# Optimization experiments

Measured on AMD Instinct MI355X. Metric: run time of the kernel, lower is better.

The kernel has to match this reference:

```python
import jax, jax.numpy as jnp
from jax import lax
import numpy as np

B, C, Hf, Wf = 4, 256, 64, 64
COMP = max(C // 4, 16)  # 64
SCALE, K_UP, K_ENC = 2, 5, 3
EPS = 1e-5


def setup_inputs() -> dict:
    key = jax.random.key(0)
    ks = jax.random.split(key, 6)
    x = jax.random.normal(ks[0], (B, C, Hf, Wf), dtype=jnp.float32)
    w_comp = jax.random.normal(ks[1], (COMP, C), dtype=jnp.float32) * (1.0 / np.sqrt(C))
    bn_gamma = jnp.ones((COMP,), dtype=jnp.float32)
    bn_beta = jnp.zeros((COMP,), dtype=jnp.float32)
    bn_mean = jax.random.normal(ks[2], (COMP,), dtype=jnp.float32) * 0.1
    bn_var = jax.random.uniform(ks[3], (COMP,), dtype=jnp.float32, minval=0.5, maxval=1.5)
    w_enc = jax.random.normal(ks[4], (K_UP * K_UP * SCALE * SCALE, COMP, K_ENC, K_ENC), dtype=jnp.float32) * (1.0 / np.sqrt(COMP * K_ENC * K_ENC))
    return {"x": x, "w_comp": w_comp, "bn_gamma": bn_gamma, "bn_beta": bn_beta,
            "bn_mean": bn_mean, "bn_var": bn_var, "w_enc": w_enc}


def reference(x, w_comp, bn_gamma, bn_beta, bn_mean, bn_var, w_enc):
    b, c, h, w = x.shape
    s, k = SCALE, K_UP
    # 1x1 compression conv
    comp = jnp.einsum('bchw,oc->bohw', x, w_comp)
    # BatchNorm (eval-style, running stats) + SiLU
    inv = (bn_gamma / jnp.sqrt(bn_var + EPS))[:, None, None]
    bn = (comp - bn_mean[:, None, None]) * inv + bn_beta[:, None, None]
    act = bn * jax.nn.sigmoid(bn)
    # encoder conv -> per-pixel reassembly kernels, channels = k^2 * s^2 (k2 outer, s2 inner)
    mask = lax.conv_general_dilated(act, w_enc, (1, 1), ((1, 1), (1, 1)),
                                    dimension_numbers=('NCHW', 'OIHW', 'NCHW'))
    mask = mask.reshape(b, k * k, s * s, h, w)
    mask = jax.nn.softmax(mask, axis=1)  # softmax over k_up*k_up window
    # unfold: gather 5x5 neighborhoods (pad 2), k = dy*5+dx row-major like F.unfold
    pad = k // 2
    xp = jnp.pad(x, ((0, 0), (0, 0), (pad, pad), (pad, pad)))
    patches = jnp.stack([xp[:, :, dy:dy + h, dx:dx + w]
                         for dy in range(k) for dx in range(k)], axis=2)  # (b,c,k2,h,w)
    # content-aware weighted sum per sub-pixel position
    out = jnp.einsum('bksij,bckij->bcsij', mask, patches)  # (b,c,s2,h,w)
    # s2 -> (s0,s1); pixel (i*s+s0, j*s+s1)
    out = out.reshape(b, c, s, s, h, w).transpose(0, 1, 4, 2, 5, 3).reshape(b, c, h * s, w * s)
    return out
```

## Files before the change

kernel.cpp:

```cpp
#include <hip/hip_runtime.h>
#include <hip/hip_bf16.h>
#include <hip/hip_fp16.h>
#include <math.h>

#define B_ 4
#define C_ 256
#define H_ 64
#define W_ 64
#define COMP_ 64
#define K2_ 25
#define HW_ (H_*W_)
#define EPS_ 1e-5f

typedef float v2f __attribute__((ext_vector_type(2)));
typedef float f32x4 __attribute__((ext_vector_type(4)));
typedef _Float16 half8 __attribute__((ext_vector_type(8)));
#define FMA2(a, b, c) __builtin_elementwise_fma((a), (b), (c))

__global__ void k_transpose(const float* __restrict__ w_comp,
                            const float* __restrict__ w_enc,
                            float* __restrict__ wTc,
                            __half* __restrict__ Apack) {
    int t = blockIdx.x * 256 + threadIdx.x;
    if (t < COMP_ * C_) {
        int o = t & 63;
        int c = t >> 6;
        wTc[t] = w_comp[o * C_ + c];
    } else {
        int t2 = t - COMP_ * C_;
        if (t2 < 8 * 18 * 64) {
            int lane = t2 & 63;
            int ks   = (t2 >> 6) % 18;
            int MT   = t2 / (64 * 18);
            int m    = MT * 16 + (lane & 15);
            __half vals[8];
#pragma unroll
            for (int e = 0; e < 8; ++e) {
                int k = ks * 32 + (lane >> 4) * 8 + e;
                int q = k >> 6;
                int c = k & 63;
                float wv = (m < 100) ? w_enc[(m * COMP_ + c) * 9 + q] : 0.f;
                vals[e] = __float2half(wv);
            }
            *(float4*)&Apack[(size_t)t2 * 8] = *(float4*)vals;
        }
    }
}

__global__ void __launch_bounds__(512)
k_compress(const float* __restrict__ x, const float* __restrict__ wTc,
           const float* __restrict__ gamma, const float* __restrict__ beta,
           const float* __restrict__ mean, const float* __restrict__ var,
           __half* __restrict__ act16) {
    __shared__ float sx[256 * 68];
    const int tx = threadIdx.x;
    const int ty = threadIdx.y;
    const int tid = ty * 64 + tx;
    const int ogu = __builtin_amdgcn_readfirstlane(ty);
    const int bb = blockIdx.y;
    const int p0 = blockIdx.x * 64;

    const float* xb = x + (size_t)bb * C_ * HW_ + p0;
#pragma unroll
    for (int l = 0; l < 8; ++l) {
        int e = tid + l * 512;
        int c = e >> 4;
        int p4 = (e & 15) << 2;
        float4 v4 = *(const float4*)(xb + (size_t)c * HW_ + p4);
        *(float4*)&sx[c * 68 + p4] = v4;
    }
    __syncthreads();

    v2f acc2[4];
#pragma unroll
    for (int k = 0; k < 4; ++k) acc2[k] = (v2f){0.f, 0.f};

#pragma unroll 8
    for (int c = 0; c < 256; ++c) {
        float xv = sx[c * 68 + tx];
        const v2f* w2 = (const v2f*)(wTc + c * COMP_ + ogu * 8);
        v2f xv2 = (v2f){xv, xv};
#pragma unroll
        for (int k = 0; k < 4; ++k)
            acc2[k] = FMA2(xv2, w2[k], acc2[k]);
    }

    __half h8[8];
#pragma unroll
    for (int k = 0; k < 4; ++k) {
#pragma unroll
        for (int h = 0; h < 2; ++h) {
            int o = ty * 8 + 2 * k + h;
            float sv = (h == 0) ? acc2[k].x : acc2[k].y;
            float iv = gamma[o] * rsqrtf(var[o] + EPS_);
            float bn = (sv - mean[o]) * iv + beta[o];
            float sg = 1.f / (1.f + __expf(-bn));
            h8[2 * k + h] = __float2half(bn * sg);
        }
    }
    __syncthreads();
    __half* sxh = (__half*)sx;
    *(float2*)&sxh[tx * 68 + ty * 8]     = *(float2*)&h8[0];
    *(float2*)&sxh[tx * 68 + ty * 8 + 4] = *(float2*)&h8[4];
    __syncthreads();

    {
        int px = tid >> 3, c8 = tid & 7;
        float2 alo = *(float2*)&sxh[px * 68 + c8 * 8];
        float2 ahi = *(float2*)&sxh[px * 68 + c8 * 8 + 4];
        float4 v = make_float4(alo.x, alo.y, ahi.x, ahi.y);
        __half* ao = act16 + ((size_t)bb * HW_ + p0 + px) * COMP_ + c8 * 8;
        *(float4*)ao = v;
    }
}

__global__ void __launch_bounds__(512)
k_encoder(const __half* __restrict__ act16, const __half* __restrict__ Apack,
          __half* __restrict__ maskT) {
    __shared__ __align__(16) __half sact[3 * 34 * 80];
    __shared__ float cbuf[32 * 129];
    __shared__ __align__(16) __half st[32 * 100];
    const int tid = threadIdx.x;
    const int i = blockIdx.x, b = blockIdx.y, jh = blockIdx.z;
    const int lane = tid & 63, w = tid >> 6;

    const __half* ab = act16 + (size_t)b * HW_ * COMP_;
    for (int t = tid; t < 3 * 34 * 8; t += 512) {
        int c8 = t & 7;
        int s  = (t >> 3) % 34;
        int r  = t / (34 * 8);
        int gi = i + r - 1;
        int gj = jh * 32 + s - 1;
        float4 v = make_float4(0.f, 0.f, 0.f, 0.f);
        if ((unsigned)gi < 64u && (unsigned)gj < 64u)
            v = *(const float4*)(ab + ((size_t)gi * 64 + gj) * COMP_ + c8 * 8);
        *(float4*)((char*)sact + (size_t)(r * 34 + s) * 160 + c8 * 16) = v;
    }
    __syncthreads();

    const int jloc0 = (w & 1) * 16;
    const int MT0   = (w >> 1) * 2;
    const int p = lane & 15, g = lane >> 4;
    f32x4 acc[2];
#pragma unroll
    for (int mt = 0; mt < 2; ++mt) acc[mt] = (f32x4){0.f, 0.f, 0.f, 0.f};
    const half8* Ap = (const half8*)Apack;
#pragma unroll
    for (int ks = 0; ks < 18; ++ks) {
        const int q = ks >> 1, ky = q / 3, kx = q % 3;
        half8 bf = *(const half8*)((const char*)sact +
                       (size_t)(ky * 34 + jloc0 + p + kx) * 160 +
                       ((ks & 1) * 32 + g * 8) * 2);
#pragma unroll
        for (int mt = 0; mt < 2; ++mt) {
            half8 af = Ap[((size_t)(MT0 + mt) * 18 + ks) * 64 + lane];
            acc[mt] = __builtin_amdgcn_mfma_f32_16x16x32_f16(af, bf, acc[mt], 0, 0, 0);
        }
    }

#pragma unroll
    for (int mt = 0; mt < 2; ++mt)
#pragma unroll
        for (int r4 = 0; r4 < 4; ++r4)
            cbuf[(jloc0 + p) * 129 + (MT0 + mt) * 16 + g * 4 + r4] = acc[mt][r4];
    __syncthreads();

    if (tid < 128) {
        int px = tid & 31, s2 = tid >> 5;
        float v[K2_];
        float mx = -1e30f;
#pragma unroll
        for (int k2 = 0; k2 < K2_; ++k2) {
            v[k2] = cbuf[px * 129 + k2 * 4 + s2];
            mx = fmaxf(mx, v[k2]);
        }
        float sum = 0.f;
#pragma unroll
        for (int k2 = 0; k2 < K2_; ++k2) { v[k2] = __expf(v[k2] - mx); sum += v[k2]; }
        float rs = 1.f / sum;
#pragma unroll
        for (int k2 = 0; k2 < K2_; ++k2)
            st[px * 100 + k2 * 4 + s2] = __float2half(v[k2] * rs);
    }
    __syncthreads();

    float4* dst = (float4*)(maskT + ((size_t)b * HW_ + i * 64 + jh * 32) * 100);
    const float4* src = (const float4*)st;
    if (tid < 400) dst[tid] = src[tid];
}

__global__ void __launch_bounds__(256)
k_reassemble(const float* __restrict__ x, const __half* __restrict__ maskT,
             float* __restrict__ out) {
    __shared__ __align__(16) __half smask[64 * 100];
    __shared__ __align__(16) float sx[5 * 68 * 20];
    const int tx = threadIdx.x;
    const int ty = threadIdx.y;
    const int tid = ty * 64 + tx;

    const int bid = blockIdx.x;
    const int id  = ((bid & 7) << 9) | (bid >> 3);
    const int cc = id & 15;
    const int i  = (id >> 4) & 63;
    const int b  = id >> 10;

    {
        const float4* src = (const float4*)(maskT + ((size_t)b * HW_ + i * 64) * 100);
        float4* dst = (float4*)smask;
#pragma unroll
        for (int t = 0; t < 4; ++t) {
            int e = tid + t * 256;
            if (e < 800) dst[e] = src[e];
        }
    }

    const float* xb = x + ((size_t)b * C_ + cc * 16 + ty * 4) * HW_;
#pragma unroll
    for (int r = 0; r < 5; ++r) {
        const int gi = i + r - 2;
        const bool rowok = ((unsigned)gi < 64u);
        {
            float4 v = {0.f, 0.f, 0.f, 0.f};
            int gj = tx - 2;
            if (rowok && gj >= 0) {
                const float* p = xb + gi * W_ + gj;
                v.x = p[0];
                v.y = p[HW_];
                v.z = p[2 * HW_];
                v.w = p[3 * HW_];
            }
            *(float4*)&sx[(r * 68 + tx) * 20 + ty * 4] = v;
        }
        if (tid < 16) {
            int q = tid >> 2;
            int col = 64 + (tid & 3);
            int gj = col - 2;
            float4 v = {0.f, 0.f, 0.f, 0.f};
            if (rowok && gj < 64) {
                const float* p = x + ((size_t)b * C_ + cc * 16 + q * 4) * HW_ + gi * W_ + gj;
                v.x = p[0];
                v.y = p[HW_];
                v.z = p[2 * HW_];
                v.w = p[3 * HW_];
            }
            *(float4*)&sx[(r * 68 + col) * 20 + q * 4] = v;
        }
    }
    __syncthreads();

    v2f a01[4], a23[4];
#pragma unroll
    for (int cl = 0; cl < 4; ++cl) { a01[cl] = (v2f){0.f, 0.f}; a23[cl] = (v2f){0.f, 0.f}; }

    float4 xq = *(const float4*)&sx[(0 * 68 + tx + 0) * 20 + ty * 4];
    float2 hm = *(const float2*)&smask[tx * 100 + 0];

#pragma unroll
    for (int k2 = 0; k2 < K2_; ++k2) {
        float4 xq_c = xq;
        float2 hm_c = hm;
        if (k2 < K2_ - 1) {
            const int kn = k2 + 1;
            const int dy = kn / 5, dx = kn % 5;
            xq = *(const float4*)&sx[(dy * 68 + tx + dx) * 20 + ty * 4];
            hm = *(const float2*)&smask[tx * 100 + kn * 4];
        }
        __half2 h01_c = ((const __half2*)&hm_c)[0];
        __half2 h23_c = ((const __half2*)&hm_c)[1];
        float2 f01 = __half22float2(h01_c);
        float2 f23 = __half22float2(h23_c);
        v2f m01 = (v2f){f01.x, f01.y};
        v2f m23 = (v2f){f23.x, f23.y};
        float xc[4] = {xq_c.x, xq_c.y, xq_c.z, xq_c.w};
#pragma unroll
        for (int cl = 0; cl < 4; ++cl) {
            v2f xv2 = (v2f){xc[cl], xc[cl]};
            a01[cl] = FMA2(xv2, m01, a01[cl]);
            a23[cl] = FMA2(xv2, m23, a23[cl]);
        }
    }

#pragma unroll
    for (int cl = 0; cl < 4; ++cl) {
        int c = cc * 16 + ty * 4 + cl;
        float* op = out + (((size_t)(b * C_ + c) * 128 + 2 * i) * 128) + 2 * tx;
        *(float2*)op         = float2{a01[cl].x, a01[cl].y};
        *(float2*)(op + 128) = float2{a23[cl].x, a23[cl].y};
    }
}

extern "C" void kernel_launch(void* const* d_in, const int* in_sizes, int n_in,
                              void* d_out, int out_size, void* d_ws, size_t ws_size,
                              hipStream_t stream) {
    const float* x       = (const float*)d_in[0];
    const float* w_comp  = (const float*)d_in[1];
    const float* bn_g    = (const float*)d_in[2];
    const float* bn_b    = (const float*)d_in[3];
    const float* bn_m    = (const float*)d_in[4];
    const float* bn_v    = (const float*)d_in[5];
    const float* w_enc   = (const float*)d_in[6];
    float* out = (float*)d_out;

    float* ws     = (float*)d_ws;
    float* wTc    = ws;
    __half* Apack = (__half*)(ws + 16384);
    __half* act16 = (__half*)(ws + 53248);
    __half* maskT = (__half*)(ws + 577536);

    k_transpose<<<100, 256, 0, stream>>>(w_comp, w_enc, wTc, Apack);
    k_compress<<<dim3(64, B_), dim3(64, 8), 0, stream>>>(x, wTc, bn_g, bn_b, bn_m, bn_v, act16);
    k_encoder<<<dim3(64, B_, 2), 512, 0, stream>>>(act16, Apack, maskT);
    k_reassemble<<<4096, dim3(64, 4), 0, stream>>>(x, maskT, out);
}
```

Baseline: 147.0 us.

## Persist reassemble blocks over channel chunks with double-buffered x tiles and reused mask

The reassemble kernel now launches 512 blocks of 512 threads. Each block handles one output row for 8 channel chunks of 16. The mask row is converted from fp16 to fp32 once into a k2-major shared layout and reused across all chunks. The x halo tile is prefetched into registers and written to a second shared buffer while the current chunk computes, which cuts redundant mask loads and overlaps global loads with FMA work. In exchange there are fewer blocks (512 on a large GPU), fewer channels per thread, more shared memory, and a serial per-block loop.

```diff
diff --git a/kernel.cpp b/kernel.cpp
--- a/kernel.cpp
+++ b/kernel.cpp
@@ -189,103 +189,121 @@
     if (tid < 400) dst[tid] = src[tid];
 }
 
-__global__ void __launch_bounds__(256)
+__global__ void __launch_bounds__(512)
 k_reassemble(const float* __restrict__ x, const __half* __restrict__ maskT,
              float* __restrict__ out) {
-    __shared__ __align__(16) __half smask[64 * 100];
-    __shared__ __align__(16) float sx[5 * 68 * 20];
+    __shared__ float maskF[K2_ * 256];
+    __shared__ float sx[2][5 * 68 * 20];
     const int tx = threadIdx.x;
     const int ty = threadIdx.y;
     const int tid = ty * 64 + tx;
 
     const int bid = blockIdx.x;
-    const int id  = ((bid & 7) << 9) | (bid >> 3);
-    const int cc = id & 15;
-    const int i  = (id >> 4) & 63;
-    const int b  = id >> 10;
-
-    {
-        const float4* src = (const float4*)(maskT + ((size_t)b * HW_ + i * 64) * 100);
-        float4* dst = (float4*)smask;
-#pragma unroll
-        for (int t = 0; t < 4; ++t) {
-            int e = tid + t * 256;
-            if (e < 800) dst[e] = src[e];
-        }
-    }
-
-    const float* xb = x + ((size_t)b * C_ + cc * 16 + ty * 4) * HW_;
-#pragma unroll
-    for (int r = 0; r < 5; ++r) {
-        const int gi = i + r - 2;
-        const bool rowok = ((unsigned)gi < 64u);
-        {
-            float4 v = {0.f, 0.f, 0.f, 0.f};
-            int gj = tx - 2;
-            if (rowok && gj >= 0) {
-                const float* p = xb + gi * W_ + gj;
-                v.x = p[0];
-                v.y = p[HW_];
-                v.z = p[2 * HW_];
-                v.w = p[3 * HW_];
-            }
-            *(float4*)&sx[(r * 68 + tx) * 20 + ty * 4] = v;
-        }
-        if (tid < 16) {
-            int q = tid >> 2;
-            int col = 64 + (tid & 3);
+    const int id  = ((bid & 7) << 6) | (bid >> 3);
+    const int half = id & 1;
+    const int i    = (id >> 1) & 63;
+    const int b    = id >> 7;
+    const int cc0  = half * 8;
+
+    float4 vx[3];
+    int offs[3];
+    auto LOADX = [&](int cc) {
+#pragma unroll
+        for (int l = 0; l < 3; ++l) {
+            int e = tid + l * 512;
+            int q = e / 340;
+            int rem = e - q * 340;
+            int r = rem / 68;
+            int col = rem - r * 68;
+            int gi = i + r - 2;
             int gj = col - 2;
-            float4 v = {0.f, 0.f, 0.f, 0.f};
-            if (rowok && gj < 64) {
+            offs[l] = (r * 68 + col) * 20 + q * 4;
+            float4 v = make_float4(0.f, 0.f, 0.f, 0.f);
+            if (e < 1360 && (unsigned)gi < 64u && (unsigned)gj < 64u) {
                 const float* p = x + ((size_t)b * C_ + cc * 16 + q * 4) * HW_ + gi * W_ + gj;
                 v.x = p[0];
                 v.y = p[HW_];
                 v.z = p[2 * HW_];
                 v.w = p[3 * HW_];
             }
-            *(float4*)&sx[(r * 68 + col) * 20 + q * 4] = v;
-        }
-    }
-    __syncthreads();
-
-    v2f a01[4], a23[4];
-#pragma unroll
-    for (int cl = 0; cl < 4; ++cl) { a01[cl] = (v2f){0.f, 0.f}; a23[cl] = (v2f){0.f, 0.f}; }
-
-    float4 xq = *(const float4*)&sx[(0 * 68 + tx + 0) * 20 + ty * 4];
-    float2 hm = *(const float2*)&smask[tx * 100 + 0];
-
-#pragma unroll
-    for (int k2 = 0; k2 < K2_; ++k2) {
-        float4 xq_c = xq;
-        float2 hm_c = hm;
-        if (k2 < K2_ - 1) {
-            const int kn = k2 + 1;
-            const int dy = kn / 5, dx = kn % 5;
-            xq = *(const float4*)&sx[(dy * 68 + tx + dx) * 20 + ty * 4];
-            hm = *(const float2*)&smask[tx * 100 + kn * 4];
-        }
-        __half2 h01_c = ((const __half2*)&hm_c)[0];
-        __half2 h23_c = ((const __half2*)&hm_c)[1];
-        float2 f01 = __half22float2(h01_c);
-        float2 f23 = __half22float2(h23_c);
-        v2f m01 = (v2f){f01.x, f01.y};
-        v2f m23 = (v2f){f23.x, f23.y};
-        float xc[4] = {xq_c.x, xq_c.y, xq_c.z, xq_c.w};
-#pragma unroll
-        for (int cl = 0; cl < 4; ++cl) {
-            v2f xv2 = (v2f){xc[cl], xc[cl]};
-            a01[cl] = FMA2(xv2, m01, a01[cl]);
-            a23[cl] = FMA2(xv2, m23, a23[cl]);
-        }
-    }
-
-#pragma unroll
-    for (int cl = 0; cl < 4; ++cl) {
-        int c = cc * 16 + ty * 4 + cl;
-        float* op = out + (((size_t)(b * C_ + c) * 128 + 2 * i) * 128) + 2 * tx;
-        *(float2*)op         = float2{a01[cl].x, a01[cl].y};
-        *(float2*)(op + 128) = float2{a23[cl].x, a23[cl].y};
+            vx[l] = v;
+        }
+    };
+    auto WRITEX = [&](int d) {
+#pragma unroll
+        for (int l = 0; l < 3; ++l) {
+            int e = tid + l * 512;
+            if (e < 1360) *(float4*)&sx[d][offs[l]] = vx[l];
+        }
+    };
+
+    LOADX(cc0);
+    {
+        const __half* mrow = maskT + ((size_t)b * HW_ + i * 64) * 100;
+#pragma unroll
+        for (int t = 0; t < 4; ++t) {
+            int f = tid + t * 512;
+            if (f < 1600) {
+                float2 raw = *(const float2*)(mrow + f * 4);
+                __half2 lo = ((const __half2*)&raw)[0];
+                __half2 hi = ((const __half2*)&raw)[1];
+                float2 flo = __half22float2(lo);
+                float2 fhi = __half22float2(hi);
+                int px = f / 25, k2 = f - px * 25;
+                *(float4*)&maskF[k2 * 256 + px * 4] =
+                    make_float4(flo.x, flo.y, fhi.x, fhi.y);
+            }
+        }
+    }
+    WRITEX(0);
+    __syncthreads();
+
+    int dbuf = 0;
+#pragma unroll 1
+    for (int n = 0; n < 8; ++n) {
+        const int cc = cc0 + n;
+        if (n < 7) LOADX(cc + 1);
+
+        const float* sb = sx[dbuf];
+        v2f a01[2], a23[2];
+#pragma unroll
+        for (int cl = 0; cl < 2; ++cl) { a01[cl] = (v2f){0.f, 0.f}; a23[cl] = (v2f){0.f, 0.f}; }
+
+        float4 mq = *(const float4*)&maskF[tx * 4];
+        float2 xv = *(const float2*)&sb[(0 * 68 + tx + 0) * 20 + ty * 2];
+#pragma unroll
+        for (int k2 = 0; k2 < K2_; ++k2) {
+            float4 mq_c = mq;
+            float2 xv_c = xv;
+            if (k2 < K2_ - 1) {
+                const int kn = k2 + 1;
+                const int dy = kn / 5, dx = kn % 5;
+                mq = *(const float4*)&maskF[kn * 256 + tx * 4];
+                xv = *(const float2*)&sb[(dy * 68 + tx + dx) * 20 + ty * 2];
+            }
+            v2f m01 = (v2f){mq_c.x, mq_c.y};
+            v2f m23 = (v2f){mq_c.z, mq_c.w};
+            float xc[2] = {xv_c.x, xv_c.y};
+#pragma unroll
+            for (int cl = 0; cl < 2; ++cl) {
+                v2f xv2 = (v2f){xc[cl], xc[cl]};
+                a01[cl] = FMA2(xv2, m01, a01[cl]);
+                a23[cl] = FMA2(xv2, m23, a23[cl]);
+            }
+        }
+
+        if (n < 7) WRITEX(dbuf ^ 1);
+
+#pragma unroll
+        for (int cl = 0; cl < 2; ++cl) {
+            int c = cc * 16 + ty * 2 + cl;
+            float* op = out + (((size_t)(b * C_ + c) * 128 + 2 * i) * 128) + 2 * tx;
+            *(float2*)op         = float2{a01[cl].x, a01[cl].y};
+            *(float2*)(op + 128) = float2{a23[cl].x, a23[cl].y};
+        }
+
+        if (n < 7) __syncthreads();
+        dbuf ^= 1;
     }
 }
 
@@ -310,5 +328,5 @@
     k_transpose<<<100, 256, 0, stream>>>(w_comp, w_enc, wTc, Apack);
     k_compress<<<dim3(64, B_), dim3(64, 8), 0, stream>>>(x, wTc, bn_g, bn_b, bn_m, bn_v, act16);
     k_encoder<<<dim3(64, B_, 2), 512, 0, stream>>>(act16, Apack, maskT);
-    k_reassemble<<<4096, dim3(64, 4), 0, stream>>>(x, maskT, out);
-}
+    k_reassemble<<<512, dim3(64, 8), 0, stream>>>(x, maskT, out);
+}
```

New measurement: 148.1 us. No clear change (+0.7%).

## Make reassembly kernel persistent with double-buffered direct global-to-LDS loads

Applied to the files above, without the earlier changes.

The reassembly kernel now launches 512 blocks, and each block loops over 8 (batch, channel-group) tiles. Each next tile's x rows and mask rows are prefetched into a second LDS buffer with global_load_lds (direct global-to-LDS DMA) while the current tile is computed. The shared-memory layout of x changes to channel-major rows with zeroed halo columns, set once per block. This trades 4096 short blocks and register-staged loads for overlapped loading, at the cost of fewer blocks in flight and a full vmcnt(0) wait plus barrier on every iteration.

```diff
diff --git a/kernel.cpp b/kernel.cpp
--- a/kernel.cpp
+++ b/kernel.cpp
@@ -16,6 +16,15 @@
 typedef float f32x4 __attribute__((ext_vector_type(4)));
 typedef _Float16 half8 __attribute__((ext_vector_type(8)));
 #define FMA2(a, b, c) __builtin_elementwise_fma((a), (b), (c))
+
+__device__ __forceinline__ void gload4(const void* g, void* l) {
+    __builtin_amdgcn_global_load_lds((const __attribute__((address_space(1))) void*)g,
+                                     (__attribute__((address_space(3))) void*)l, 4, 0, 0);
+}
+__device__ __forceinline__ void gload16(const void* g, void* l) {
+    __builtin_amdgcn_global_load_lds((const __attribute__((address_space(1))) void*)g,
+                                     (__attribute__((address_space(3))) void*)l, 16, 0, 0);
+}
 
 __global__ void k_transpose(const float* __restrict__ w_comp,
                             const float* __restrict__ w_enc,
@@ -192,100 +201,107 @@
 __global__ void __launch_bounds__(256)
 k_reassemble(const float* __restrict__ x, const __half* __restrict__ maskT,
              float* __restrict__ out) {
-    __shared__ __align__(16) __half smask[64 * 100];
-    __shared__ __align__(16) float sx[5 * 68 * 20];
+    __shared__ float sxp[2][5][16][68];
+    __shared__ __align__(16) __half smaskp[2][6400];
     const int tx = threadIdx.x;
     const int ty = threadIdx.y;
     const int tid = ty * 64 + tx;
 
     const int bid = blockIdx.x;
-    const int id  = ((bid & 7) << 9) | (bid >> 3);
-    const int cc = id & 15;
-    const int i  = (id >> 4) & 63;
-    const int b  = id >> 10;
-
-    {
-        const float4* src = (const float4*)(maskT + ((size_t)b * HW_ + i * 64) * 100);
-        float4* dst = (float4*)smask;
-#pragma unroll
-        for (int t = 0; t < 4; ++t) {
-            int e = tid + t * 256;
-            if (e < 800) dst[e] = src[e];
-        }
-    }
-
-    const float* xb = x + ((size_t)b * C_ + cc * 16 + ty * 4) * HW_;
+    const int xcd = bid & 7;
+    const int kk  = bid >> 3;
+    const int i   = xcd * 8 + (kk & 7);
+    const int bc  = kk >> 3;
+
+    for (int e = tid; e < 640; e += 256) {
+        int d = e / 320; int rem = e - d * 320;
+        int r = rem >> 6; int rem2 = rem & 63;
+        int c = rem2 >> 2; int q = rem2 & 3;
+        int col = (q & 1) + (q >> 1) * 66;
+        sxp[d][r][c][col] = 0.f;
+    }
 #pragma unroll
     for (int r = 0; r < 5; ++r) {
-        const int gi = i + r - 2;
-        const bool rowok = ((unsigned)gi < 64u);
-        {
-            float4 v = {0.f, 0.f, 0.f, 0.f};
-            int gj = tx - 2;
-            if (rowok && gj >= 0) {
-                const float* p = xb + gi * W_ + gj;
-                v.x = p[0];
-                v.y = p[HW_];
-                v.z = p[2 * HW_];
-                v.w = p[3 * HW_];
-            }
-            *(float4*)&sx[(r * 68 + tx) * 20 + ty * 4] = v;
-        }
-        if (tid < 16) {
-            int q = tid >> 2;
-            int col = 64 + (tid & 3);
-            int gj = col - 2;
-            float4 v = {0.f, 0.f, 0.f, 0.f};
-            if (rowok && gj < 64) {
-                const float* p = x + ((size_t)b * C_ + cc * 16 + q * 4) * HW_ + gi * W_ + gj;
-                v.x = p[0];
-                v.y = p[HW_];
-                v.z = p[2 * HW_];
-                v.w = p[3 * HW_];
-            }
-            *(float4*)&sx[(r * 68 + col) * 20 + q * 4] = v;
-        }
-    }
-    __syncthreads();
-
-    v2f a01[4], a23[4];
-#pragma unroll
-    for (int cl = 0; cl < 4; ++cl) { a01[cl] = (v2f){0.f, 0.f}; a23[cl] = (v2f){0.f, 0.f}; }
-
-    float4 xq = *(const float4*)&sx[(0 * 68 + tx + 0) * 20 + ty * 4];
-    float2 hm = *(const float2*)&smask[tx * 100 + 0];
-
-#pragma unroll
-    for (int k2 = 0; k2 < K2_; ++k2) {
-        float4 xq_c = xq;
-        float2 hm_c = hm;
-        if (k2 < K2_ - 1) {
-            const int kn = k2 + 1;
-            const int dy = kn / 5, dx = kn % 5;
-            xq = *(const float4*)&sx[(dy * 68 + tx + dx) * 20 + ty * 4];
-            hm = *(const float2*)&smask[tx * 100 + kn * 4];
-        }
-        __half2 h01_c = ((const __half2*)&hm_c)[0];
-        __half2 h23_c = ((const __half2*)&hm_c)[1];
-        float2 f01 = __half22float2(h01_c);
-        float2 f23 = __half22float2(h23_c);
-        v2f m01 = (v2f){f01.x, f01.y};
-        v2f m23 = (v2f){f23.x, f23.y};
-        float xc[4] = {xq_c.x, xq_c.y, xq_c.z, xq_c.w};
+        int gi = i + r - 2;
+        if ((unsigned)gi >= 64u) {
+            for (int e = tid; e < 2 * 16 * 68; e += 256) {
+                int d = e / 1088; int rem = e - d * 1088;
+                int c = rem / 68; int col = rem - c * 68;
+                sxp[d][r][c][col] = 0.f;
+            }
+        }
+    }
+
+    auto stage = [&](int n, int d) {
+        const int b  = n >> 1;
+        const int cc = bc * 2 + (n & 1);
+        const float* xit = x + ((size_t)b * C_ + cc * 16) * HW_;
+#pragma unroll
+        for (int r = 0; r < 5; ++r) {
+            int gi = i + r - 2;
+            if ((unsigned)gi < 64u) {
+#pragma unroll
+                for (int c4 = 0; c4 < 4; ++c4) {
+                    int c = (ty << 2) + c4;
+                    gload4(xit + (size_t)c * HW_ + gi * W_ + tx, &sxp[d][r][c][2]);
+                }
+            }
+        }
+        const char* mrow = (const char*)(maskT + ((size_t)b * HW_ + i * 64) * 100);
+        char* mdst = (char*)&smaskp[d][0];
+        if (ty < 3) {
+#pragma unroll
+            for (int m = 0; m < 4; ++m) {
+                int mi = ty * 4 + m;
+                gload16(mrow + mi * 1024 + tx * 16, mdst + mi * 1024);
+            }
+        } else {
+            gload4(mrow + 12288 + tx * 4, mdst + 12288);
+            gload4(mrow + 12544 + tx * 4, mdst + 12544);
+        }
+    };
+
+    stage(0, 0);
+
+#pragma unroll 1
+    for (int n = 0; n < 8; ++n) {
+        const int d = n & 1;
+        asm volatile("s_waitcnt vmcnt(0)" ::: "memory");
+        __syncthreads();
+        if (n + 1 < 8) stage(n + 1, d ^ 1);
+
+        const int b  = n >> 1;
+        const int cc = bc * 2 + (n & 1);
+
+        v2f a01[4], a23[4];
+#pragma unroll
+        for (int cl = 0; cl < 4; ++cl) { a01[cl] = (v2f){0.f, 0.f}; a23[cl] = (v2f){0.f, 0.f}; }
+
+#pragma unroll
+        for (int k2 = 0; k2 < K2_; ++k2) {
+            const int dy = k2 / 5, dx = k2 % 5;
+            __half2 h01 = *(const __half2*)&smaskp[d][tx * 100 + k2 * 4];
+            __half2 h23 = *(const __half2*)&smaskp[d][tx * 100 + k2 * 4 + 2];
+            float2 f01 = __half22float2(h01);
+            float2 f23 = __half22float2(h23);
+            v2f m01 = (v2f){f01.x, f01.y};
+            v2f m23 = (v2f){f23.x, f23.y};
+#pragma unroll
+            for (int cl = 0; cl < 4; ++cl) {
+                float xv = sxp[d][dy][(ty << 2) + cl][tx + dx];
+                v2f xv2 = (v2f){xv, xv};
+                a01[cl] = FMA2(xv2, m01, a01[cl]);
+                a23[cl] = FMA2(xv2, m23, a23[cl]);
+            }
+        }
+
 #pragma unroll
         for (int cl = 0; cl < 4; ++cl) {
-            v2f xv2 = (v2f){xc[cl], xc[cl]};
-            a01[cl] = FMA2(xv2, m01, a01[cl]);
-            a23[cl] = FMA2(xv2, m23, a23[cl]);
-        }
-    }
-
-#pragma unroll
-    for (int cl = 0; cl < 4; ++cl) {
-        int c = cc * 16 + ty * 4 + cl;
-        float* op = out + (((size_t)(b * C_ + c) * 128 + 2 * i) * 128) + 2 * tx;
-        *(float2*)op         = float2{a01[cl].x, a01[cl].y};
-        *(float2*)(op + 128) = float2{a23[cl].x, a23[cl].y};
+            int c = cc * 16 + (ty << 2) + cl;
+            float* op = out + (((size_t)(b * C_ + c) * 128 + 2 * i) * 128) + 2 * tx;
+            *(float2*)op         = float2{a01[cl].x, a01[cl].y};
+            *(float2*)(op + 128) = float2{a23[cl].x, a23[cl].y};
+        }
     }
 }
 
@@ -310,5 +326,5 @@
     k_transpose<<<100, 256, 0, stream>>>(w_comp, w_enc, wTc, Apack);
     k_compress<<<dim3(64, B_), dim3(64, 8), 0, stream>>>(x, wTc, bn_g, bn_b, bn_m, bn_v, act16);
     k_encoder<<<dim3(64, B_, 2), 512, 0, stream>>>(act16, Apack, maskT);
-    k_reassemble<<<4096, dim3(64, 4), 0, stream>>>(x, maskT, out);
-}
+    k_reassemble<<<512, dim3(64, 4), 0, stream>>>(x, maskT, out);
+}
```

Result: faster. 141.3 us (-3.9%).
